# Optimization experiments

Hardware: AMD Instinct MI355X
Metric: run time of the kernel (lower is better)

## Reference

```python
import jax, jax.numpy as jnp
import numpy as np

N_NODES = 10000
NUM_GENE = 2000
N_EDGES = 160000
HEADS = 10
HID = 128          # GAT layer1 out_channels
LATENT = 128
LOWER = 64
CLUSTERS = 15
SIGMA = 0.5
NEG_SLOPE = 0.2


def gat_conv(x, src, dst, W, a_src, a_dst, b, concat):
    """PyG GATConv (eval mode, self-loops already appended to src/dst).
    x: [N, Fin]; W: [Fin, H*D]; a_src/a_dst: [H, D]; b: [H*D] or [D]."""
    N = x.shape[0]
    H, D = a_src.shape
    h = (x @ W).reshape(N, H, D)                       # [N,H,D]
    e_s = jnp.einsum('nhd,hd->nh', h, a_src)           # [N,H]
    e_d = jnp.einsum('nhd,hd->nh', h, a_dst)
    alpha = jax.nn.leaky_relu(e_s[src] + e_d[dst], NEG_SLOPE)   # [E,H]
    m = jax.ops.segment_max(alpha, dst, num_segments=N)          # [N,H]
    p = jnp.exp(alpha - m[dst])
    s = jax.ops.segment_sum(p, dst, num_segments=N)
    w = p / s[dst]                                     # segment softmax [E,H]
    out = jax.ops.segment_sum(h[src] * w[:, :, None], dst, num_segments=N)  # [N,H,D]
    out = out.reshape(N, H * D) if concat else out.mean(axis=1)
    return out + b


def add_self_loops(edge_index, n):
    loop = jnp.arange(n, dtype=edge_index.dtype)
    src = jnp.concatenate([edge_index[0], loop])
    dst = jnp.concatenate([edge_index[1], loop])
    return src, dst


def setup_inputs() -> dict:
    key = jax.random.key(0)
    ks = jax.random.split(key, 20)
    g = lambda k, shape, fan: jax.random.normal(k, shape, jnp.float32) * (1.0 / np.sqrt(fan))
    inp = {
        'x': jax.random.normal(ks[0], (N_NODES, NUM_GENE), jnp.float32),
        'edge_index': jax.random.randint(ks[1], (2, N_EDGES), 0, N_NODES, dtype=jnp.int32),
        'noise': jax.random.normal(ks[2], (N_NODES, NUM_GENE), jnp.float32) * SIGMA,
        # GAT layer 1: in=NUM_GENE, out=HID, heads=HEADS, concat
        'W1': g(ks[3], (NUM_GENE, HEADS * HID), NUM_GENE),
        'a1_src': g(ks[4], (HEADS, HID), HID),
        'a1_dst': g(ks[5], (HEADS, HID), HID),
        'b1': jnp.zeros((HEADS * HID,), jnp.float32),
        # GAT layer 2: in=HEADS*HID, out=LATENT, heads=HEADS, mean
        'W2': g(ks[6], (HEADS * HID, HEADS * LATENT), HEADS * HID),
        'a2_src': g(ks[7], (HEADS, LATENT), LATENT),
        'a2_dst': g(ks[8], (HEADS, LATENT), LATENT),
        'b2': jnp.zeros((LATENT,), jnp.float32),
        # MLP
        'Wm1': g(ks[9], (NUM_GENE, LATENT), NUM_GENE),
        'bm1': jnp.zeros((LATENT,), jnp.float32),
        'Wm2': g(ks[10], (LATENT, LATENT), LATENT),
        'bm2': jnp.zeros((LATENT,), jnp.float32),
        # projection heads
        'Wf': g(ks[11], (LATENT, LOWER), LATENT),
        'bf': jnp.zeros((LOWER,), jnp.float32),
        'Wc': g(ks[12], (LATENT, CLUSTERS), LATENT),
        'bc': jnp.zeros((CLUSTERS,), jnp.float32),
    }
    return inp


def reference(x, edge_index, noise, W1, a1_src, a1_dst, b1, W2, a2_src, a2_dst, b2,
              Wm1, bm1, Wm2, bm2, Wf, bf, Wc, bc):
    N = x.shape[0]
    src, dst = add_self_loops(edge_index, N)

    # x_aug = x + F.normalize(noise, dim=1)
    nrm = jnp.sqrt(jnp.sum(noise * noise, axis=1, keepdims=True))
    x_aug = x + noise / jnp.maximum(nrm, 1e-12)

    def gat_enc(inp):
        h1 = jax.nn.relu(gat_conv(inp, src, dst, W1, a1_src, a1_dst, b1, concat=True))
        h2 = jax.nn.relu(gat_conv(h1, src, dst, W2, a2_src, a2_dst, b2, concat=False))
        return h2

    gx = gat_enc(x)          # [N, LATENT]
    gx1 = gat_enc(x_aug)
    gx2 = (jax.nn.relu(x @ Wm1 + bm1)) @ Wm2 + bm2   # MLP

    g0 = gx.mean(axis=0)     # global avg pooling -> [LATENT]
    g1 = gx1.mean(axis=0)
    g2 = gx2.mean(axis=0)

    T = 0.2
    e01 = jnp.exp(jnp.dot(g0, g1) / T)
    e02 = jnp.exp(jnp.dot(g0, g2) / T)
    e12 = jnp.exp(jnp.dot(g1, g2) / T)
    loss_graph = -jnp.log10(e01 / (e01 + e02 + e12))

    gx_node = gx @ Wf + bf
    gx1_node = gx1 @ Wf + bf
    gx2_node = gx2 @ Wf + bf
    gx_c = (gx @ Wc + bc).T      # [CLUSTERS, N]
    gx1_c = (gx1 @ Wc + bc).T
    return (gx_node, gx1_node, gx2_node, loss_graph, gx_c, gx1_c)
```

## Files before the change

### kernel.cpp

```cpp
#include <hip/hip_runtime.h>
#include <hip/hip_bf16.h>

#define N_NODESC 10000
#define M_PAD    10112
#define RT_TILES 79
#define NUM_GENE 2000
#define KPAD_G   2048
#define N_EDGESC 160000
#define E_TOT    170000
#define HEADS    10
#define F1       1280
#define LATENTC  128
#define LOWERC   64
#define CLUST    15

typedef __attribute__((ext_vector_type(8))) short   short8;
typedef __attribute__((ext_vector_type(4))) float   f32x4;
typedef __attribute__((ext_vector_type(4))) unsigned short ushort4_;

__device__ __forceinline__ float bf2f(unsigned short u){
    unsigned int x = ((unsigned int)u) << 16;
    return __builtin_bit_cast(float, x);
}
__device__ __forceinline__ unsigned short f2bf(float f){
    __hip_bfloat16 h = __float2bfloat16(f);
    return __builtin_bit_cast(unsigned short, h);
}
__device__ __forceinline__ void gload16(const void* g, void* l) {
    __builtin_amdgcn_global_load_lds((const __attribute__((address_space(1))) void*)g,
                                     (__attribute__((address_space(3))) void*)l, 16, 0, 0);
}

template<int OMODE>
__global__ __launch_bounds__(512, 2)
void gemm256(const unsigned short* __restrict__ A, int lda,
             const unsigned short* __restrict__ BT, int ldb,
             void* __restrict__ Cp, int ldc,
             int NK, int NT, int M_real)
{
    __shared__ short smem[65536];

    const int nwg = gridDim.x;
    const int q = nwg >> 3, r = nwg & 7;
    const int xcd = blockIdx.x & 7, idx = blockIdx.x >> 3;
    const int wgid = (xcd < r ? xcd * (q + 1) : r * (q + 1) + (xcd - r) * q) + idx;
    const int bm = wgid / NT, bn = wgid - bm * NT;

    const int t = threadIdx.x, w = t >> 6, lane = t & 63;
    const int wr2 = (w >> 2) * 64;
    const int wc2 = (w & 3) * 32;
    const int lrow = lane & 15, lq = lane >> 4;

    int rowc[2], swc[2], loff[2];
    #pragma unroll
    for (int cc = 0; cc < 2; ++cc) {
        int c = cc * 512 + t;
        int row = c >> 3, slot = c & 7;
        rowc[cc] = row;
        swc[cc]  = (slot ^ (row & 7)) << 3;
        loff[cc] = c * 8;
    }
    auto stageA = [&](int buf, int h, int kt) {
        short* dst = smem + buf * 32768 + h * 8192;
        const unsigned short* src = A + (size_t)(bm * 256 + h * 128) * lda + kt * 64;
        #pragma unroll
        for (int cc = 0; cc < 2; ++cc)
            gload16(src + (size_t)rowc[cc] * lda + swc[cc], dst + loff[cc]);
    };
    auto stageB = [&](int buf, int h, int kt) {
        short* dst = smem + buf * 32768 + 16384 + h * 8192;
        const unsigned short* src = BT + (size_t)(bn * 256 + h * 128) * ldb + kt * 64;
        #pragma unroll
        for (int cc = 0; cc < 2; ++cc)
            gload16(src + (size_t)rowc[cc] * ldb + swc[cc], dst + loff[cc]);
    };
    auto rdA = [&](int buf, int h, int mi, int ks) -> short8 {
        int r7 = wr2 + mi * 16 + lrow;
        return *(const short8*)(smem + buf * 32768 + h * 8192 + r7 * 64
                                + (((ks * 4 + lq) ^ (r7 & 7)) << 3));
    };
    auto rdB = [&](int buf, int h, int ni, int ks) -> short8 {
        int r7 = wc2 + ni * 16 + lrow;
        return *(const short8*)(smem + buf * 32768 + 16384 + h * 8192 + r7 * 64
                                + (((ks * 4 + lq) ^ (r7 & 7)) << 3));
    };

    f32x4 acc00[4][2] = {}, acc01[4][2] = {}, acc10[4][2] = {}, acc11[4][2] = {};
    short8 a0[4][2], a1[4][2], b0[2][2], b1[2][2];

    auto domfma = [&](f32x4 (&ac)[4][2], short8 (&aa)[4][2], short8 (&bb)[2][2]) {
        __builtin_amdgcn_s_setprio(1);
        #pragma unroll
        for (int mi = 0; mi < 4; ++mi)
            #pragma unroll
            for (int ni = 0; ni < 2; ++ni)
                #pragma unroll
                for (int ks = 0; ks < 2; ++ks)
                    ac[mi][ni] = __builtin_amdgcn_mfma_f32_16x16x32_bf16(
                        aa[mi][ks], bb[ni][ks], ac[mi][ni], 0, 0, 0);
        __builtin_amdgcn_s_setprio(0);
    };

    stageA(0, 0, 0); stageB(0, 0, 0); stageB(0, 1, 0); stageA(0, 1, 0);

    for (int kt = 0; kt < NK; ++kt) {
        const int buf = kt & 1, nbuf = buf ^ 1;
        const bool pf = (kt + 1 < NK);
        asm volatile("s_waitcnt vmcnt(4)" ::: "memory");
        __builtin_amdgcn_sched_barrier(0);
        __builtin_amdgcn_s_barrier();
        __builtin_amdgcn_sched_barrier(0);
        if (pf) stageA(nbuf, 0, kt + 1);
        #pragma unroll
        for (int mi = 0; mi < 4; ++mi) { a0[mi][0] = rdA(buf, 0, mi, 0); a0[mi][1] = rdA(buf, 0, mi, 1); }
        #pragma unroll
        for (int ni = 0; ni < 2; ++ni) { b0[ni][0] = rdB(buf, 0, ni, 0); b0[ni][1] = rdB(buf, 0, ni, 1); }
        domfma(acc00, a0, b0);
        if (pf) { asm volatile("s_waitcnt vmcnt(4)" ::: "memory"); }
        else    { asm volatile("s_waitcnt vmcnt(2)" ::: "memory"); }
        __builtin_amdgcn_sched_barrier(0);
        __builtin_amdgcn_s_barrier();
        __builtin_amdgcn_sched_barrier(0);
        if (pf) stageB(nbuf, 0, kt + 1);
        #pragma unroll
        for (int ni = 0; ni < 2; ++ni) { b1[ni][0] = rdB(buf, 1, ni, 0); b1[ni][1] = rdB(buf, 1, ni, 1); }
        domfma(acc01, a0, b1);
        if (pf) { asm volatile("s_waitcnt vmcnt(4)" ::: "memory"); }
        else    { asm volatile("s_waitcnt vmcnt(0)" ::: "memory"); }
        __builtin_amdgcn_sched_barrier(0);
        __builtin_amdgcn_s_barrier();
        __builtin_amdgcn_sched_barrier(0);
        if (pf) stageB(nbuf, 1, kt + 1);
        #pragma unroll
        for (int mi = 0; mi < 4; ++mi) { a1[mi][0] = rdA(buf, 1, mi, 0); a1[mi][1] = rdA(buf, 1, mi, 1); }
        domfma(acc10, a1, b0);
        if (pf) stageA(nbuf, 1, kt + 1);
        domfma(acc11, a1, b1);
    }

    #pragma unroll
    for (int qa = 0; qa < 2; ++qa) {
        #pragma unroll
        for (int qb = 0; qb < 2; ++qb) {
            f32x4 (&ac)[4][2] = (qa == 0) ? (qb == 0 ? acc00 : acc01)
                                          : (qb == 0 ? acc10 : acc11);
            #pragma unroll
            for (int mi = 0; mi < 4; ++mi) {
                #pragma unroll
                for (int ni = 0; ni < 2; ++ni) {
                    int gcol = bn * 256 + qb * 128 + wc2 + ni * 16 + lrow;
                    #pragma unroll
                    for (int qq = 0; qq < 4; ++qq) {
                        int grow = bm * 256 + qa * 128 + wr2 + mi * 16 + lq * 4 + qq;
                        float val = ac[mi][ni][qq];
                        int rslab = grow >= M_PAD ? grow - M_PAD : grow;
                        if (rslab >= M_real) val = 0.f;
                        if constexpr (OMODE == 0)
                            ((unsigned short*)Cp)[(size_t)grow * ldc + gcol] = f2bf(val);
                        else
                            ((float*)Cp)[(size_t)grow * ldc + gcol] = val;
                    }
                }
            }
        }
    }
}

template<int OMODE, int BIAS, int RELU>
__global__ __launch_bounds__(256)
void gemm2(const unsigned short* __restrict__ A, int lda,
           const unsigned short* __restrict__ BT, int ldb,
           const float* __restrict__ bias,
           void* __restrict__ Cp, int ldc,
           int KT, int NT, int M_real, int NSPLIT, int slab)
{
    __shared__ short smem[16384];

    const int nwg = gridDim.x;
    const int q = nwg >> 3, r = nwg & 7;
    const int xcd = blockIdx.x & 7, idx = blockIdx.x >> 3;
    const int wgid = (xcd < r ? xcd * (q + 1) : r * (q + 1) + (xcd - r) * q) + idx;
    const int tot_mn = nwg / NSPLIT;
    const int s  = wgid / tot_mn;
    const int mn = wgid - s * tot_mn;
    const int bm = mn / NT, bn = mn - bm * NT;

    const int t = threadIdx.x, w = t >> 6, lane = t & 63;
    const int wr = (w >> 1) * 64, wc = (w & 1) * 64;
    const int lrow = lane & 15, lq = lane >> 4;

    const int kt_beg = s * KT, kt_end = kt_beg + KT;

    const unsigned short* Ag[2];
    const unsigned short* Bg[2];
    int lds_off[2];
    #pragma unroll
    for (int cc = 0; cc < 2; ++cc) {
        int c = cc * 256 + t;
        int row = c >> 2, slot = c & 3;
        int gk = (slot ^ ((row >> 1) & 3)) << 3;
        Ag[cc] = A  + (size_t)(bm * 128 + row) * lda + gk;
        Bg[cc] = BT + (size_t)(bn * 128 + row) * ldb + gk;
        lds_off[cc] = cc * 2048 + w * 512 + lane * 8;
    }

    auto stage = [&](int buf, int kt) {
        const int kk = kt * 32;
        #pragma unroll
        for (int cc = 0; cc < 2; ++cc) {
            gload16(Ag[cc] + kk, smem + buf * 8192 + lds_off[cc]);
            gload16(Bg[cc] + kk, smem + buf * 8192 + 4096 + lds_off[cc]);
        }
    };

    f32x4 acc[4][4] = {};
    stage(0, kt_beg);
    __syncthreads();
    int cur = 0;
    for (int kt = kt_beg; kt < kt_end; ++kt) {
        if (kt + 1 < kt_end) stage(cur ^ 1, kt + 1);
        const short* As = smem + cur * 8192;
        const short* Bs = As + 4096;
        short8 af[4], bf_[4];
        #pragma unroll
        for (int mi = 0; mi < 4; ++mi) {
            int rr = wr + mi * 16 + lrow;
            af[mi] = *(const short8*)(&As[rr * 32 + ((lq ^ ((rr >> 1) & 3)) << 3)]);
        }
        #pragma unroll
        for (int ni = 0; ni < 4; ++ni) {
            int rr = wc + ni * 16 + lrow;
            bf_[ni] = *(const short8*)(&Bs[rr * 32 + ((lq ^ ((rr >> 1) & 3)) << 3)]);
        }
        #pragma unroll
        for (int mi = 0; mi < 4; ++mi)
            #pragma unroll
            for (int ni = 0; ni < 4; ++ni)
                acc[mi][ni] = __builtin_amdgcn_mfma_f32_16x16x32_bf16(af[mi], bf_[ni], acc[mi][ni], 0, 0, 0);
        __syncthreads();
        cur ^= 1;
    }

    float* Cf = (float*)Cp + (size_t)s * slab;
    #pragma unroll
    for (int mi = 0; mi < 4; ++mi) {
        #pragma unroll
        for (int ni = 0; ni < 4; ++ni) {
            int gcol = bn * 128 + wc + ni * 16 + lrow;
            #pragma unroll
            for (int qq = 0; qq < 4; ++qq) {
                int grow = bm * 128 + wr + mi * 16 + lq * 4 + qq;
                float val = acc[mi][ni][qq];
                if constexpr (OMODE == 2) {
                    Cf[(size_t)grow * ldc + gcol] = val;
                } else {
                    if constexpr (BIAS) val += bias[gcol];
                    if constexpr (RELU) val = fmaxf(val, 0.f);
                    if (grow >= M_real) val = 0.f;
                    ((float*)Cp)[(size_t)grow * ldc + gcol] = val;
                }
            }
        }
    }
}

__global__ void convert_both_k(const float* __restrict__ x, const float* __restrict__ noise,
                               unsigned short* __restrict__ out)
{
    __shared__ float sred[4];
    __shared__ float srn;
    int row = blockIdx.x, t = threadIdx.x;
    int kc = t * 8;
    f32x4 n0 = {}, n1 = {};
    float ss = 0.f;
    if (t < 250) {
        n0 = *(const f32x4*)(noise + (size_t)row * NUM_GENE + kc);
        n1 = *(const f32x4*)(noise + (size_t)row * NUM_GENE + kc + 4);
        ss = n0.x*n0.x + n0.y*n0.y + n0.z*n0.z + n0.w*n0.w
           + n1.x*n1.x + n1.y*n1.y + n1.z*n1.z + n1.w*n1.w;
    }
    for (int off = 32; off; off >>= 1) ss += __shfl_down(ss, off);
    if ((t & 63) == 0) sred[t >> 6] = ss;
    __syncthreads();
    if (t == 0) srn = 1.f / fmaxf(sqrtf(sred[0] + sred[1] + sred[2] + sred[3]), 1e-12f);
    __syncthreads();
    if (t >= 250) return;
    float rn = srn;
    f32x4 a0 = *(const f32x4*)(x + (size_t)row * NUM_GENE + kc);
    f32x4 a1 = *(const f32x4*)(x + (size_t)row * NUM_GENE + kc + 4);
    short8 v0, v1;
    #pragma unroll
    for (int i = 0; i < 4; ++i) {
        v0[i]     = (short)f2bf(a0[i]);
        v0[4 + i] = (short)f2bf(a1[i]);
        v1[i]     = (short)f2bf(a0[i] + n0[i] * rn);
        v1[4 + i] = (short)f2bf(a1[i] + n1[i] * rn);
    }
    *(short8*)(out + (size_t)row * KPAD_G + kc) = v0;
    *(short8*)(out + (size_t)(M_PAD + row) * KPAD_G + kc) = v1;
}

__global__ void splitred_k(const float* __restrict__ part, const float* __restrict__ bm1,
                           unsigned short* __restrict__ out)
{
    int gid = blockIdx.x * 256 + threadIdx.x;
    int row = gid >> 5, c4 = (gid & 31) * 4;
    if (row >= N_NODESC) return;
    size_t o = (size_t)row * 128 + c4;
    const size_t slab = (size_t)M_PAD * 128;
    f32x4 v = *(const f32x4*)(part + o) + *(const f32x4*)(part + slab + o)
            + *(const f32x4*)(part + 2 * slab + o) + *(const f32x4*)(part + 3 * slab + o);
    f32x4 b = *(const f32x4*)(bm1 + c4);
    ushort4_ u;
    u.x = f2bf(fmaxf(v.x + b.x, 0.f)); u.y = f2bf(fmaxf(v.y + b.y, 0.f));
    u.z = f2bf(fmaxf(v.z + b.z, 0.f)); u.w = f2bf(fmaxf(v.w + b.w, 0.f));
    *(ushort4_*)(out + o) = u;
}

__global__ void transpose_bf_k(const float* __restrict__ in, unsigned short* __restrict__ out,
                               int R, int C, int Kpad)
{
    __shared__ float tile[32][33];
    int tx = threadIdx.x & 31, ty = threadIdx.x >> 5;
    int c0 = blockIdx.x * 32, r0 = blockIdx.y * 32;
    #pragma unroll
    for (int i = 0; i < 4; ++i) {
        int r = r0 + ty + i * 8, c = c0 + tx;
        tile[ty + i * 8][tx] = (r < R && c < C) ? in[(size_t)r * C + c] : 0.f;
    }
    __syncthreads();
    #pragma unroll
    for (int i = 0; i < 4; ++i) {
        int c = c0 + ty + i * 8;
        int r = r0 + tx;
        if (c < C && r < Kpad) out[(size_t)c * Kpad + r] = f2bf(tile[tx][ty + i * 8]);
    }
}

__global__ void hist_k(const int* __restrict__ ei, int* __restrict__ cnt)
{
    int e = blockIdx.x * 256 + threadIdx.x;
    if (e >= E_TOT) return;
    int d = (e < N_EDGESC) ? ei[N_EDGESC + e] : (e - N_EDGESC);
    atomicAdd(&cnt[d], 1);
}

__global__ void scan_k(const int* __restrict__ cnt, int* __restrict__ rowp, int* __restrict__ cursor)
{
    __shared__ int buf[1024];
    int t = threadIdx.x;
    int loc[10];
    int s = 0, base = t * 10;
    #pragma unroll
    for (int i = 0; i < 10; ++i) {
        int idx = base + i;
        int v = (idx < N_NODESC) ? cnt[idx] : 0;
        loc[i] = v; s += v;
    }
    buf[t] = s; __syncthreads();
    for (int off = 1; off < 1024; off <<= 1) {
        int tmp = (t >= off) ? buf[t - off] : 0;
        __syncthreads();
        buf[t] += tmp;
        __syncthreads();
    }
    int run = buf[t] - s;
    #pragma unroll
    for (int i = 0; i < 10; ++i) {
        int idx = base + i;
        if (idx < N_NODESC) { rowp[idx] = run; cursor[idx] = run; run += loc[i]; }
    }
    if (t == 1023) rowp[N_NODESC] = buf[1023];
}

__global__ void scatter_k(const int* __restrict__ ei, int* __restrict__ cursor,
                          int* __restrict__ col_src, int* __restrict__ dst_of)
{
    int e = blockIdx.x * 256 + threadIdx.x;
    if (e >= E_TOT) return;
    int s, d;
    if (e < N_EDGESC) { s = ei[e]; d = ei[N_EDGESC + e]; } else { s = d = e - N_EDGESC; }
    int pos = atomicAdd(&cursor[d], 1);
    col_src[pos] = s;
    dst_of[pos] = d;
}

__global__ void escores2_k(const unsigned short* __restrict__ h,
                           const float* __restrict__ a_src, const float* __restrict__ a_dst,
                           float* __restrict__ e_s, float* __restrict__ e_d)
{
    int t = threadIdx.x;
    int half = (t >= 160);
    int tl = t - half * 160;
    int node2 = blockIdx.x * 2 + half;
    int p = node2 >= N_NODESC;
    int n = node2 - p * N_NODESC;
    int hh = tl >> 4, c = tl & 15;
    int off = hh * 128 + c * 8;
    short8 v = *(const short8*)(h + (size_t)(p * M_PAD + n) * F1 + off);
    float ps = 0.f, pd = 0.f;
    #pragma unroll
    for (int j = 0; j < 8; ++j) {
        float f = bf2f((unsigned short)v[j]);
        ps += f * a_src[off + j];
        pd += f * a_dst[off + j];
    }
    #pragma unroll
    for (int m = 1; m < 16; m <<= 1) {
        ps += __shfl_xor(ps, m, 16);
        pd += __shfl_xor(pd, m, 16);
    }
    if (c == 0) { e_s[node2 * HEADS + hh] = ps; e_d[node2 * HEADS + hh] = pd; }
}

__global__ void alpha_k(const int* __restrict__ colsrc, const int* __restrict__ dstof,
                        const float* __restrict__ e_s, const float* __restrict__ e_d,
                        float* __restrict__ alpha)
{
    int gid = blockIdx.x * 256 + threadIdx.x;
    if (gid >= 2 * E_TOT) return;
    int p = gid >= E_TOT;
    int e = gid - p * E_TOT;
    int s = colsrc[e], d = dstof[e];
    const float* er = e_s + (size_t)(p * N_NODESC + s) * HEADS;
    const float* dr = e_d + (size_t)(p * N_NODESC + d) * HEADS;
    #pragma unroll
    for (int h = 0; h < HEADS; ++h) {
        float a = er[h] + dr[h];
        a = a >= 0.f ? a : 0.2f * a;
        alpha[((size_t)p * HEADS + h) * E_TOT + e] = a;
    }
}

__global__ void nodems_k(const int* __restrict__ rowp, const float* __restrict__ alpha,
                         float2* __restrict__ minv)
{
    int gid = blockIdx.x * 256 + threadIdx.x;
    if (gid >= 2 * N_NODESC * HEADS) return;
    int p = gid >= N_NODESC * HEADS;
    int rr = gid - p * N_NODESC * HEADS;
    int n = rr / HEADS, hh = rr - n * HEADS;
    int beg = rowp[n], end = rowp[n + 1];
    const float* ap = alpha + ((size_t)p * HEADS + hh) * E_TOT;
    float m = -1e30f, ssum = 0.f;
    for (int e = beg; e < end; ++e) {
        float a = ap[e];
        if (a > m) { ssum = ssum * __expf(m - a) + 1.f; m = a; }
        else ssum += __expf(a - m);
    }
    float2 qo; qo.x = m; qo.y = 1.f / ssum;
    minv[gid] = qo;
}

__global__ void wexp_k(const int* __restrict__ dstof, const float2* __restrict__ minv,
                       float* __restrict__ alpha)
{
    int gid = blockIdx.x * 256 + threadIdx.x;
    if (gid >= 2 * E_TOT) return;
    int p = gid >= E_TOT;
    int e = gid - p * E_TOT;
    int d = dstof[e];
    const float2* mv = minv + (size_t)(p * N_NODESC + d) * HEADS;
    #pragma unroll
    for (int h = 0; h < HEADS; ++h) {
        float2 qv = mv[h];
        size_t o = ((size_t)p * HEADS + h) * E_TOT + e;
        alpha[o] = __expf(alpha[o] - qv.x) * qv.y;
    }
}

template<int L1MODE>
__global__ void agg_slice_k(const int* __restrict__ rowp, const int* __restrict__ colsrc,
                            const float* __restrict__ alpha,
                            const unsigned short* __restrict__ h,
                            const float* __restrict__ bias,
                            unsigned short* __restrict__ out)
{
    const int nwg = gridDim.x;
    const int q = nwg >> 3, r = nwg & 7;
    const int xcd = blockIdx.x & 7, idx = blockIdx.x >> 3;
    const int wgid = (xcd < r ? xcd * (q + 1) : r * (q + 1) + (xcd - r) * q) + idx;
    int ps = wgid / 625, nb = wgid - ps * 625;
    int p = ps / HEADS, s = ps - p * HEADS;
    int t = threadIdx.x;
    int nl = t >> 4, l16 = t & 15;
    int n = nb * 16 + nl;
    int beg = rowp[n], end = rowp[n + 1];
    const unsigned short* hb = h + (size_t)p * M_PAD * F1 + s * 128 + l16 * 8;
    const float* wb = alpha + ((size_t)p * HEADS + s) * E_TOT;
    float acc[8] = {};
    for (int e = beg; e < end; ++e) {
        int src = colsrc[e];
        float wv = wb[e];
        short8 rv = *(const short8*)(hb + (size_t)src * F1);
        #pragma unroll
        for (int j = 0; j < 8; ++j) acc[j] += wv * bf2f((unsigned short)rv[j]);
    }
    short8 o;
    if constexpr (L1MODE) {
        #pragma unroll
        for (int j = 0; j < 8; ++j)
            o[j] = (short)f2bf(fmaxf(acc[j] + bias[s * 128 + l16 * 8 + j], 0.f));
    } else {
        #pragma unroll
        for (int j = 0; j < 8; ++j) o[j] = (short)f2bf(acc[j]);
    }
    *(short8*)(out + (size_t)(p * M_PAD + n) * F1 + s * 128 + l16 * 8) = o;
}

__global__ void headmean_k(const unsigned short* __restrict__ tmp, const float* __restrict__ b2,
                           float* __restrict__ out)
{
    int gid = blockIdx.x * 256 + threadIdx.x;
    int pn = gid >> 4, d8 = (gid & 15) * 8;
    int p = pn >= N_NODESC;
    int n = pn - p * N_NODESC;
    const unsigned short* tp = tmp + (size_t)(p * M_PAD + n) * F1 + d8;
    float acc[8] = {};
    #pragma unroll
    for (int hh = 0; hh < HEADS; ++hh) {
        short8 v = *(const short8*)(tp + hh * 128);
        #pragma unroll
        for (int j = 0; j < 8; ++j) acc[j] += bf2f((unsigned short)v[j]);
    }
    float* op = out + (size_t)(p * M_PAD + n) * LATENTC + d8;
    #pragma unroll
    for (int j = 0; j < 8; ++j) op[j] = fmaxf(acc[j] * 0.1f + b2[d8 + j], 0.f);
}

__global__ void colsum_k(const float* __restrict__ g01, const float* __restrict__ g2,
                         float* __restrict__ gsum)
{
    int v = blockIdx.x / 40, b = blockIdx.x % 40;
    const float* src = (v == 0) ? g01 : (v == 1) ? g01 + (size_t)M_PAD * 128 : g2;
    int t = threadIdx.x, col = t & 127, ro = t >> 7;
    int rend = min((b + 1) * 250, N_NODESC);
    float acc = 0.f;
    for (int r = b * 250 + ro; r < rend; r += 2) acc += src[(size_t)r * 128 + col];
    __shared__ float part[256];
    part[t] = acc; __syncthreads();
    if (t < 128) atomicAdd(&gsum[v * 128 + col], part[t] + part[t + 128]);
}

__global__ void loss_k(const float* __restrict__ gsum, float* __restrict__ out)
{
    int t = threadIdx.x;
    float g0 = gsum[t] * 1e-4f, g1 = gsum[128 + t] * 1e-4f, g2 = gsum[256 + t] * 1e-4f;
    float d01 = g0 * g1, d02 = g0 * g2, d12 = g1 * g2;
    for (int off = 32; off; off >>= 1) {
        d01 += __shfl_down(d01, off); d02 += __shfl_down(d02, off); d12 += __shfl_down(d12, off);
    }
    __shared__ float s[3][2];
    if ((t & 63) == 0) { int w = t >> 6; s[0][w] = d01; s[1][w] = d02; s[2][w] = d12; }
    __syncthreads();
    if (t == 0) {
        float a01 = (s[0][0] + s[0][1]) * 5.f;
        float a02 = (s[1][0] + s[1][1]) * 5.f;
        float a12 = (s[2][0] + s[2][1]) * 5.f;
        float m = fmaxf(a01, fmaxf(a02, a12));
        float se = expf(a01 - m) + expf(a02 - m) + expf(a12 - m);
        *out = -((a01 - m) - logf(se)) / 2.302585092994046f;
    }
}

__global__ void proj_k(const float* __restrict__ g01, const float* __restrict__ g2,
                       const float* __restrict__ Wf, const float* __restrict__ bfv,
                       const float* __restrict__ Wc, const float* __restrict__ bc,
                       float* __restrict__ out)
{
    __shared__ float rowb[4][128];
    int m = blockIdx.y;
    const float* gx = (m == 0) ? g01 : (m == 1) ? g01 + (size_t)M_PAD * 128 : g2;
    float* out_node = out + (size_t)m * 640000;
    float* out_c = (m == 0) ? out + 1920001 : (m == 1) ? out + 2070001 : nullptr;
    int wid = threadIdx.x >> 6, l = threadIdx.x & 63;
    int n = blockIdx.x * 4 + wid;
    if (n >= N_NODESC) return;
    rowb[wid][l]      = gx[(size_t)n * 128 + l];
    rowb[wid][l + 64] = gx[(size_t)n * 128 + 64 + l];
    float acc = bfv[l];
    #pragma unroll 8
    for (int k = 0; k < 128; ++k) acc += rowb[wid][k] * Wf[k * 64 + l];
    out_node[(size_t)n * 64 + l] = acc;
    if (out_c != nullptr && l < CLUST) {
        float a2 = bc[l];
        #pragma unroll 8
        for (int k = 0; k < 128; ++k) a2 += rowb[wid][k] * Wc[k * CLUST + l];
        out_c[(size_t)l * N_NODESC + n] = a2;
    }
}

extern "C" void kernel_launch(void* const* d_in, const int* in_sizes, int n_in,
                              void* d_out, int out_size, void* d_ws, size_t ws_size,
                              hipStream_t stream)
{
    const float* x     = (const float*)d_in[0];
    const int*   ei    = (const int*)  d_in[1];
    const float* noise = (const float*)d_in[2];
    const float* W1    = (const float*)d_in[3];
    const float* a1s   = (const float*)d_in[4];
    const float* a1d   = (const float*)d_in[5];
    const float* b1    = (const float*)d_in[6];
    const float* W2    = (const float*)d_in[7];
    const float* a2s   = (const float*)d_in[8];
    const float* a2d   = (const float*)d_in[9];
    const float* b2    = (const float*)d_in[10];
    const float* Wm1   = (const float*)d_in[11];
    const float* bm1   = (const float*)d_in[12];
    const float* Wm2   = (const float*)d_in[13];
    const float* bm2   = (const float*)d_in[14];
    const float* Wf    = (const float*)d_in[15];
    const float* bfv   = (const float*)d_in[16];
    const float* Wc    = (const float*)d_in[17];
    const float* bc    = (const float*)d_in[18];
    float* out = (float*)d_out;

    size_t off = 0;
    auto alloc = [&](size_t bytes) { size_t o = off; off = (off + bytes + 255) & ~(size_t)255; return o; };
    char* ws = (char*)d_ws;
    unsigned short* xbuf2  = (unsigned short*)(ws + alloc((size_t)2 * M_PAD * KPAD_G * 2));
    unsigned short* hraw2  = (unsigned short*)(ws + alloc((size_t)2 * M_PAD * F1 * 2));
    unsigned short* w1t    = (unsigned short*)(ws + alloc((size_t)F1 * KPAD_G * 2));
    unsigned short* w2t    = (unsigned short*)(ws + alloc((size_t)F1 * F1 * 2));
    unsigned short* wm1t   = (unsigned short*)(ws + alloc((size_t)128 * KPAD_G * 2));
    unsigned short* wm2t   = (unsigned short*)(ws + alloc((size_t)128 * 128 * 2));
    unsigned short* t_bf   = (unsigned short*)(ws + alloc((size_t)M_PAD * 128 * 2));
    float*  alpha  = (float*) (ws + alloc((size_t)2 * E_TOT * HEADS * 4));
    float2* minv   = (float2*)(ws + alloc((size_t)2 * N_NODESC * HEADS * 8));
    float*  es     = (float*) (ws + alloc((size_t)2 * N_NODESC * HEADS * 4));
    float*  edv    = (float*) (ws + alloc((size_t)2 * N_NODESC * HEADS * 4));
    int*    cnt    = (int*)   (ws + alloc((size_t)N_NODESC * 4));
    int*    rowp   = (int*)   (ws + alloc((size_t)(N_NODESC + 16) * 4));
    int*    cursor = (int*)   (ws + alloc((size_t)N_NODESC * 4));
    int*    colsrc = (int*)   (ws + alloc((size_t)E_TOT * 4));
    int*    dstof  = (int*)   (ws + alloc((size_t)E_TOT * 4));
    float*  gx01   = (float*) (ws + alloc((size_t)2 * M_PAD * 128 * 4));
    float*  gx2    = (float*) (ws + alloc((size_t)M_PAD * 128 * 4));
    float*  gsum   = (float*) (ws + alloc((size_t)384 * 4));
    unsigned short* h1x2 = xbuf2;
    unsigned short* tmp2 = xbuf2;
    float* gxpart = (float*)hraw2;
    (void)ws_size; (void)in_sizes; (void)n_in; (void)out_size;

    hipMemsetAsync(cnt, 0, (size_t)N_NODESC * 4, stream);
    hipMemsetAsync(gsum, 0, 384 * 4, stream);

    convert_both_k<<<N_NODESC, 256, 0, stream>>>(x, noise, xbuf2);

    transpose_bf_k<<<dim3(40, 64), 256, 0, stream>>>(W1,  w1t,  NUM_GENE, F1,  KPAD_G);
    transpose_bf_k<<<dim3(40, 40), 256, 0, stream>>>(W2,  w2t,  F1,       F1,  F1);
    transpose_bf_k<<<dim3(4, 64),  256, 0, stream>>>(Wm1, wm1t, NUM_GENE, 128, KPAD_G);
    transpose_bf_k<<<dim3(4, 4),   256, 0, stream>>>(Wm2, wm2t, 128,      128, 128);

    hist_k   <<<(E_TOT + 255) / 256, 256, 0, stream>>>(ei, cnt);
    scan_k   <<<1, 1024, 0, stream>>>(cnt, rowp, cursor);
    scatter_k<<<(E_TOT + 255) / 256, 256, 0, stream>>>(ei, cursor, colsrc, dstof);

    gemm2<2,0,0><<<RT_TILES * 4, 256, 0, stream>>>(xbuf2, KPAD_G, wm1t, KPAD_G,
        nullptr, gxpart, 128, 16, 1, N_NODESC, 4, M_PAD * 128);
    splitred_k<<<1250, 256, 0, stream>>>(gxpart, bm1, t_bf);
    gemm2<1,1,0><<<RT_TILES, 256, 0, stream>>>(t_bf, 128, wm2t, 128,
        bm2, gx2, 128, 4, 1, N_NODESC, 1, 0);

    gemm256<0><<<RT_TILES * 5, 512, 0, stream>>>(xbuf2, KPAD_G, w1t, KPAD_G,
        hraw2, F1, 32, 5, N_NODESC);
    escores2_k<<<N_NODESC, 320, 0, stream>>>(hraw2, a1s, a1d, es, edv);
    alpha_k <<<(2 * E_TOT + 255) / 256, 256, 0, stream>>>(colsrc, dstof, es, edv, alpha);
    nodems_k<<<(2 * N_NODESC * HEADS + 255) / 256, 256, 0, stream>>>(rowp, alpha, minv);
    wexp_k  <<<(2 * E_TOT + 255) / 256, 256, 0, stream>>>(dstof, minv, alpha);
    agg_slice_k<1><<<12500, 256, 0, stream>>>(rowp, colsrc, alpha, hraw2, b1, h1x2);

    gemm256<0><<<RT_TILES * 5, 512, 0, stream>>>(h1x2, F1, w2t, F1,
        hraw2, F1, 20, 5, N_NODESC);
    escores2_k<<<N_NODESC, 320, 0, stream>>>(hraw2, a2s, a2d, es, edv);
    alpha_k <<<(2 * E_TOT + 255) / 256, 256, 0, stream>>>(colsrc, dstof, es, edv, alpha);
    nodems_k<<<(2 * N_NODESC * HEADS + 255) / 256, 256, 0, stream>>>(rowp, alpha, minv);
    wexp_k  <<<(2 * E_TOT + 255) / 256, 256, 0, stream>>>(dstof, minv, alpha);
    agg_slice_k<0><<<12500, 256, 0, stream>>>(rowp, colsrc, alpha, hraw2, nullptr, tmp2);
    headmean_k<<<1250, 256, 0, stream>>>(tmp2, b2, gx01);

    colsum_k<<<120, 256, 0, stream>>>(gx01, gx2, gsum);
    loss_k  <<<1, 128, 0, stream>>>(gsum, out + 1920000);

    proj_k<<<dim3(2500, 3), 256, 0, stream>>>(gx01, gx2, Wf, bfv, Wc, bc, out);
}
```

Measured before the change: 683.7 us.

## Fold MLP first layer into GAT layer-1 GEMM as extra N tile

Appends the transposed Wm1 (padded with zeros to 256 columns) to W1's transposed buffer so the big 256x256 GEMM computes both x@W1 and x@Wm1 in one launch. The last N tile applies bias and ReLU and writes bf16 MLP hidden activations, which removes the split-K gemm2 launch and the splitred reduction kernel. It also moves the LDS fragment reads ahead of the next-stage global prefetch in the main loop. The cost is wasted MFMA work on 128 zero-padded columns in the extra tile, and the MLP tile reads both x and x_aug rows even though only the x rows are needed.

```diff
diff --git a/kernel.cpp b/kernel.cpp
--- a/kernel.cpp
+++ b/kernel.cpp
@@ -31,12 +31,13 @@
                                      (__attribute__((address_space(3))) void*)l, 16, 0, 0);
 }
 
-template<int OMODE>
+template<int OMODE, int FOLD>
 __global__ __launch_bounds__(512, 2)
 void gemm256(const unsigned short* __restrict__ A, int lda,
              const unsigned short* __restrict__ BT, int ldb,
              void* __restrict__ Cp, int ldc,
-             int NK, int NT, int M_real)
+             int NK, int NT, int M_real,
+             const float* __restrict__ mbias, unsigned short* __restrict__ mout)
 {
     __shared__ short smem[65536];
 
@@ -110,40 +111,60 @@
         __builtin_amdgcn_sched_barrier(0);
         __builtin_amdgcn_s_barrier();
         __builtin_amdgcn_sched_barrier(0);
+        #pragma unroll
+        for (int mi = 0; mi < 4; ++mi) { a0[mi][0] = rdA(buf, 0, mi, 0); a0[mi][1] = rdA(buf, 0, mi, 1); }
+        #pragma unroll
+        for (int ni = 0; ni < 2; ++ni) { b0[ni][0] = rdB(buf, 0, ni, 0); b0[ni][1] = rdB(buf, 0, ni, 1); }
         if (pf) stageA(nbuf, 0, kt + 1);
-        #pragma unroll
-        for (int mi = 0; mi < 4; ++mi) { a0[mi][0] = rdA(buf, 0, mi, 0); a0[mi][1] = rdA(buf, 0, mi, 1); }
-        #pragma unroll
-        for (int ni = 0; ni < 2; ++ni) { b0[ni][0] = rdB(buf, 0, ni, 0); b0[ni][1] = rdB(buf, 0, ni, 1); }
         domfma(acc00, a0, b0);
         if (pf) { asm volatile("s_waitcnt vmcnt(4)" ::: "memory"); }
         else    { asm volatile("s_waitcnt vmcnt(2)" ::: "memory"); }
         __builtin_amdgcn_sched_barrier(0);
         __builtin_amdgcn_s_barrier();
         __builtin_amdgcn_sched_barrier(0);
+        #pragma unroll
+        for (int ni = 0; ni < 2; ++ni) { b1[ni][0] = rdB(buf, 1, ni, 0); b1[ni][1] = rdB(buf, 1, ni, 1); }
         if (pf) stageB(nbuf, 0, kt + 1);
-        #pragma unroll
-        for (int ni = 0; ni < 2; ++ni) { b1[ni][0] = rdB(buf, 1, ni, 0); b1[ni][1] = rdB(buf, 1, ni, 1); }
         domfma(acc01, a0, b1);
         if (pf) { asm volatile("s_waitcnt vmcnt(4)" ::: "memory"); }
         else    { asm volatile("s_waitcnt vmcnt(0)" ::: "memory"); }
         __builtin_amdgcn_sched_barrier(0);
         __builtin_amdgcn_s_barrier();
         __builtin_amdgcn_sched_barrier(0);
+        #pragma unroll
+        for (int mi = 0; mi < 4; ++mi) { a1[mi][0] = rdA(buf, 1, mi, 0); a1[mi][1] = rdA(buf, 1, mi, 1); }
         if (pf) stageB(nbuf, 1, kt + 1);
-        #pragma unroll
-        for (int mi = 0; mi < 4; ++mi) { a1[mi][0] = rdA(buf, 1, mi, 0); a1[mi][1] = rdA(buf, 1, mi, 1); }
         domfma(acc10, a1, b0);
         if (pf) stageA(nbuf, 1, kt + 1);
         domfma(acc11, a1, b1);
     }
 
+    const bool mlp_tile = FOLD && (bn == NT - 1);
     #pragma unroll
     for (int qa = 0; qa < 2; ++qa) {
         #pragma unroll
         for (int qb = 0; qb < 2; ++qb) {
             f32x4 (&ac)[4][2] = (qa == 0) ? (qb == 0 ? acc00 : acc01)
                                           : (qb == 0 ? acc10 : acc11);
+            if (mlp_tile) {
+                if (qb != 0) continue;
+                #pragma unroll
+                for (int mi = 0; mi < 4; ++mi) {
+                    #pragma unroll
+                    for (int ni = 0; ni < 2; ++ni) {
+                        int col = wc2 + ni * 16 + lrow;
+                        #pragma unroll
+                        for (int qq = 0; qq < 4; ++qq) {
+                            int grow = bm * 256 + qa * 128 + wr2 + mi * 16 + lq * 4 + qq;
+                            if (grow < N_NODESC) {
+                                float val = fmaxf(ac[mi][ni][qq] + mbias[col], 0.f);
+                                mout[(size_t)grow * 128 + col] = f2bf(val);
+                            }
+                        }
+                    }
+                }
+                continue;
+            }
             #pragma unroll
             for (int mi = 0; mi < 4; ++mi) {
                 #pragma unroll
@@ -172,7 +193,7 @@
            const unsigned short* __restrict__ BT, int ldb,
            const float* __restrict__ bias,
            void* __restrict__ Cp, int ldc,
-           int KT, int NT, int M_real, int NSPLIT, int slab)
+           int KT, int NT, int M_real)
 {
     __shared__ short smem[16384];
 
@@ -180,16 +201,11 @@
     const int q = nwg >> 3, r = nwg & 7;
     const int xcd = blockIdx.x & 7, idx = blockIdx.x >> 3;
     const int wgid = (xcd < r ? xcd * (q + 1) : r * (q + 1) + (xcd - r) * q) + idx;
-    const int tot_mn = nwg / NSPLIT;
-    const int s  = wgid / tot_mn;
-    const int mn = wgid - s * tot_mn;
-    const int bm = mn / NT, bn = mn - bm * NT;
+    const int bm = wgid / NT, bn = wgid - bm * NT;
 
     const int t = threadIdx.x, w = t >> 6, lane = t & 63;
     const int wr = (w >> 1) * 64, wc = (w & 1) * 64;
     const int lrow = lane & 15, lq = lane >> 4;
-
-    const int kt_beg = s * KT, kt_end = kt_beg + KT;
 
     const unsigned short* Ag[2];
     const unsigned short* Bg[2];
@@ -214,11 +230,11 @@
     };
 
     f32x4 acc[4][4] = {};
-    stage(0, kt_beg);
+    stage(0, 0);
     __syncthreads();
     int cur = 0;
-    for (int kt = kt_beg; kt < kt_end; ++kt) {
-        if (kt + 1 < kt_end) stage(cur ^ 1, kt + 1);
+    for (int kt = 0; kt < KT; ++kt) {
+        if (kt + 1 < KT) stage(cur ^ 1, kt + 1);
         const short* As = smem + cur * 8192;
         const short* Bs = As + 4096;
         short8 af[4], bf_[4];
@@ -241,7 +257,6 @@
         cur ^= 1;
     }
 
-    float* Cf = (float*)Cp + (size_t)s * slab;
     #pragma unroll
     for (int mi = 0; mi < 4; ++mi) {
         #pragma unroll
@@ -251,14 +266,10 @@
             for (int qq = 0; qq < 4; ++qq) {
                 int grow = bm * 128 + wr + mi * 16 + lq * 4 + qq;
                 float val = acc[mi][ni][qq];
-                if constexpr (OMODE == 2) {
-                    Cf[(size_t)grow * ldc + gcol] = val;
-                } else {
-                    if constexpr (BIAS) val += bias[gcol];
-                    if constexpr (RELU) val = fmaxf(val, 0.f);
-                    if (grow >= M_real) val = 0.f;
-                    ((float*)Cp)[(size_t)grow * ldc + gcol] = val;
-                }
+                if constexpr (BIAS) val += bias[gcol];
+                if constexpr (RELU) val = fmaxf(val, 0.f);
+                if (grow >= M_real) val = 0.f;
+                ((float*)Cp)[(size_t)grow * ldc + gcol] = val;
             }
         }
     }
@@ -298,23 +309,6 @@
     }
     *(short8*)(out + (size_t)row * KPAD_G + kc) = v0;
     *(short8*)(out + (size_t)(M_PAD + row) * KPAD_G + kc) = v1;
-}
-
-__global__ void splitred_k(const float* __restrict__ part, const float* __restrict__ bm1,
-                           unsigned short* __restrict__ out)
-{
-    int gid = blockIdx.x * 256 + threadIdx.x;
-    int row = gid >> 5, c4 = (gid & 31) * 4;
-    if (row >= N_NODESC) return;
-    size_t o = (size_t)row * 128 + c4;
-    const size_t slab = (size_t)M_PAD * 128;
-    f32x4 v = *(const f32x4*)(part + o) + *(const f32x4*)(part + slab + o)
-            + *(const f32x4*)(part + 2 * slab + o) + *(const f32x4*)(part + 3 * slab + o);
-    f32x4 b = *(const f32x4*)(bm1 + c4);
-    ushort4_ u;
-    u.x = f2bf(fmaxf(v.x + b.x, 0.f)); u.y = f2bf(fmaxf(v.y + b.y, 0.f));
-    u.z = f2bf(fmaxf(v.z + b.z, 0.f)); u.w = f2bf(fmaxf(v.w + b.w, 0.f));
-    *(ushort4_*)(out + o) = u;
 }
 
 __global__ void transpose_bf_k(const float* __restrict__ in, unsigned short* __restrict__ out,
@@ -620,9 +614,8 @@
     char* ws = (char*)d_ws;
     unsigned short* xbuf2  = (unsigned short*)(ws + alloc((size_t)2 * M_PAD * KPAD_G * 2));
     unsigned short* hraw2  = (unsigned short*)(ws + alloc((size_t)2 * M_PAD * F1 * 2));
-    unsigned short* w1t    = (unsigned short*)(ws + alloc((size_t)F1 * KPAD_G * 2));
+    unsigned short* w1t    = (unsigned short*)(ws + alloc((size_t)1536 * KPAD_G * 2));
     unsigned short* w2t    = (unsigned short*)(ws + alloc((size_t)F1 * F1 * 2));
-    unsigned short* wm1t   = (unsigned short*)(ws + alloc((size_t)128 * KPAD_G * 2));
     unsigned short* wm2t   = (unsigned short*)(ws + alloc((size_t)128 * 128 * 2));
     unsigned short* t_bf   = (unsigned short*)(ws + alloc((size_t)M_PAD * 128 * 2));
     float*  alpha  = (float*) (ws + alloc((size_t)2 * E_TOT * HEADS * 4));
@@ -639,39 +632,36 @@
     float*  gsum   = (float*) (ws + alloc((size_t)384 * 4));
     unsigned short* h1x2 = xbuf2;
     unsigned short* tmp2 = xbuf2;
-    float* gxpart = (float*)hraw2;
     (void)ws_size; (void)in_sizes; (void)n_in; (void)out_size;
 
     hipMemsetAsync(cnt, 0, (size_t)N_NODESC * 4, stream);
     hipMemsetAsync(gsum, 0, 384 * 4, stream);
+    hipMemsetAsync(w1t + (size_t)1408 * KPAD_G, 0, (size_t)128 * KPAD_G * 2, stream);
 
     convert_both_k<<<N_NODESC, 256, 0, stream>>>(x, noise, xbuf2);
 
     transpose_bf_k<<<dim3(40, 64), 256, 0, stream>>>(W1,  w1t,  NUM_GENE, F1,  KPAD_G);
+    transpose_bf_k<<<dim3(4, 64),  256, 0, stream>>>(Wm1, w1t + (size_t)1280 * KPAD_G, NUM_GENE, 128, KPAD_G);
     transpose_bf_k<<<dim3(40, 40), 256, 0, stream>>>(W2,  w2t,  F1,       F1,  F1);
-    transpose_bf_k<<<dim3(4, 64),  256, 0, stream>>>(Wm1, wm1t, NUM_GENE, 128, KPAD_G);
     transpose_bf_k<<<dim3(4, 4),   256, 0, stream>>>(Wm2, wm2t, 128,      128, 128);
 
     hist_k   <<<(E_TOT + 255) / 256, 256, 0, stream>>>(ei, cnt);
     scan_k   <<<1, 1024, 0, stream>>>(cnt, rowp, cursor);
     scatter_k<<<(E_TOT + 255) / 256, 256, 0, stream>>>(ei, cursor, colsrc, dstof);
 
-    gemm2<2,0,0><<<RT_TILES * 4, 256, 0, stream>>>(xbuf2, KPAD_G, wm1t, KPAD_G,
-        nullptr, gxpart, 128, 16, 1, N_NODESC, 4, M_PAD * 128);
-    splitred_k<<<1250, 256, 0, stream>>>(gxpart, bm1, t_bf);
+    gemm256<0,1><<<RT_TILES * 6, 512, 0, stream>>>(xbuf2, KPAD_G, w1t, KPAD_G,
+        hraw2, F1, 32, 6, N_NODESC, bm1, t_bf);
     gemm2<1,1,0><<<RT_TILES, 256, 0, stream>>>(t_bf, 128, wm2t, 128,
-        bm2, gx2, 128, 4, 1, N_NODESC, 1, 0);
-
-    gemm256<0><<<RT_TILES * 5, 512, 0, stream>>>(xbuf2, KPAD_G, w1t, KPAD_G,
-        hraw2, F1, 32, 5, N_NODESC);
+        bm2, gx2, 128, 4, 1, N_NODESC);
+
     escores2_k<<<N_NODESC, 320, 0, stream>>>(hraw2, a1s, a1d, es, edv);
     alpha_k <<<(2 * E_TOT + 255) / 256, 256, 0, stream>>>(colsrc, dstof, es, edv, alpha);
     nodems_k<<<(2 * N_NODESC * HEADS + 255) / 256, 256, 0, stream>>>(rowp, alpha, minv);
     wexp_k  <<<(2 * E_TOT + 255) / 256, 256, 0, stream>>>(dstof, minv, alpha);
     agg_slice_k<1><<<12500, 256, 0, stream>>>(rowp, colsrc, alpha, hraw2, b1, h1x2);
 
-    gemm256<0><<<RT_TILES * 5, 512, 0, stream>>>(h1x2, F1, w2t, F1,
-        hraw2, F1, 20, 5, N_NODESC);
+    gemm256<0,0><<<RT_TILES * 5, 512, 0, stream>>>(h1x2, F1, w2t, F1,
+        hraw2, F1, 20, 5, N_NODESC, nullptr, nullptr);
     escores2_k<<<N_NODESC, 320, 0, stream>>>(hraw2, a2s, a2d, es, edv);
     alpha_k <<<(2 * E_TOT + 255) / 256, 256, 0, stream>>>(colsrc, dstof, es, edv, alpha);
     nodems_k<<<(2 * N_NODESC * HEADS + 255) / 256, 256, 0, stream>>>(rowp, alpha, minv);
```

Result: faster. 662.2 us (-3.1%).
